# Performance work log

Measured on AMD Instinct MI355X. Metric: run time of the kernel, lower is better.

Reference implementation:

```python
import jax, jax.numpy as jnp
import numpy as np

N_NODES = 50000
N_EDGES = 600000
N_DISCRETE = 70
NH = N_DISCRETE - 6          # 64
EMB = 128                    # n_embedding
D = NH + EMB                 # 192, resdnn/cross input dim
RES_HID = 512                # l_hidden entries
N_RES = 2                    # len(l_hidden)
N_CROSS = 2
PRED_HID = (2 * NH + 512) // 2  # 320
NEG_SLOPE = 0.01


def setup_inputs() -> dict:
    key = jax.random.key(0)
    ks = jax.random.split(key, 24)
    def w(k, shape, fan_in):
        return (jax.random.normal(k, shape, jnp.float32) / np.sqrt(fan_in)).astype(jnp.float32)
    inp = {
        "discrete_x": jax.random.randint(ks[0], (N_NODES, N_DISCRETE), 0, 100, jnp.int64),
        "edge_index": jax.random.randint(ks[1], (2, N_EDGES), 0, N_NODES, jnp.int64),
        # graph embedding linear + 2 GCN layers
        "w_g0": w(ks[2], (NH, EMB), NH), "b_g0": jnp.zeros((EMB,), jnp.float32),
        "w_gcn1": w(ks[3], (EMB, EMB), EMB), "b_gcn1": jnp.zeros((EMB,), jnp.float32),
        "w_gcn2": w(ks[4], (EMB, EMB), EMB), "b_gcn2": jnp.zeros((EMB,), jnp.float32),
        # ResDNN: N_RES dim-preserving residual bottleneck blocks D->RES_HID->D
        "res_w1": w(ks[5], (N_RES, D, RES_HID), D), "res_b1": jnp.zeros((N_RES, RES_HID), jnp.float32),
        "res_w2": w(ks[6], (N_RES, RES_HID, D), RES_HID), "res_b2": jnp.zeros((N_RES, D), jnp.float32),
        # CrossNet: N_CROSS layers
        "cross_w": w(ks[7], (N_CROSS, D), D), "cross_b": jnp.zeros((N_CROSS, D), jnp.float32),
        # Prediction MLP: 2D -> PRED_HID -> 1, sigmoid
        "p_w1": w(ks[8], (2 * D, PRED_HID), 2 * D), "p_b1": jnp.zeros((PRED_HID,), jnp.float32),
        "p_w2": w(ks[9], (PRED_HID, 1), PRED_HID), "p_b2": jnp.zeros((1,), jnp.float32),
    }
    return inp


def _leaky(x):
    return jax.nn.leaky_relu(x, NEG_SLOPE)


def _gcn_conv(x, W, b, row, col, n):
    # PyG GCNConv: linear, then sym-normalized aggregation over A + I, then bias
    h = x @ W
    deg = jax.ops.segment_sum(jnp.ones(row.shape, x.dtype), col, num_segments=n) + 1.0
    dinv = jax.lax.rsqrt(deg)
    norm = dinv[row] * dinv[col]            # [E]
    msg = h[row] * norm[:, None]            # [E, EMB]  (largest intermediate)
    agg = jax.ops.segment_sum(msg, col, num_segments=n)
    agg = agg + h * (dinv * dinv)[:, None]  # self-loop contribution
    return agg + b


def reference(discrete_x, edge_index, w_g0, b_g0, w_gcn1, b_gcn1, w_gcn2, b_gcn2,
              res_w1, res_b1, res_w2, res_b2, cross_w, cross_b,
              p_w1, p_b1, p_w2, p_b2):
    n = discrete_x.shape[0]
    row, col = edge_index[0], edge_index[1]
    # DiscreteFeatureEmbeddingLayer: map n_discrete_features int cols -> nh float dims
    x_d = discrete_x[:, :NH].astype(jnp.float32)
    # graph branch
    x_g = _leaky(x_d @ w_g0 + b_g0)
    x_g = _leaky(_gcn_conv(x_g, w_gcn1, b_gcn1, row, col, n))
    x_g = _leaky(_gcn_conv(x_g, w_gcn2, b_gcn2, row, col, n))
    x = jnp.concatenate([x_d, x_g], axis=-1)  # [N, D]
    # ResDNN: residual bottleneck blocks
    x_deep = x
    for i in range(N_RES):
        h = _leaky(x_deep @ res_w1[i] + res_b1[i])
        x_deep = _leaky(x_deep + h @ res_w2[i] + res_b2[i])
    # CrossNet (DCN): x_{l+1} = x0 * (x_l . w_l) + b_l + x_l
    x0 = x
    x_cross = x
    for i in range(N_CROSS):
        xw = x_cross @ cross_w[i]            # [N]
        x_cross = x0 * xw[:, None] + cross_b[i] + x_cross
    z = jnp.concatenate([x_deep, x_cross], axis=-1)  # [N, 2D]
    h = _leaky(z @ p_w1 + p_b1)
    y = jax.nn.sigmoid(h @ p_w2 + p_b2)
    return y.squeeze(-1)
```

## Files before the change

### kernel.cpp

```cpp
#include <hip/hip_runtime.h>
#include <math.h>

constexpr int NCOLS   = 70;
constexpr int NH      = 64;
constexpr int EMB     = 128;
constexpr int DD      = 192;
constexpr int RES_HID = 512;
constexpr int PRED_HID= 320;

typedef _Float16 f16x8 __attribute__((ext_vector_type(8)));
typedef float    f32x4 __attribute__((ext_vector_type(4)));
#define MFMA16F(a,b,c) __builtin_amdgcn_mfma_f32_16x16x32_f16((a),(b),(c),0,0,0)

constexpr float LO_SCALE   = 4096.0f;
constexpr float LO_DESCALE = 1.0f/4096.0f;
constexpr float Z_SCALE    = 0.0625f;
constexpr float Z_DESCALE  = 16.0f;

__device__ __forceinline__ float leaky(float x){ return x > 0.f ? x : 0.01f*x; }

__global__ void k_hist(const int* __restrict__ col, int* __restrict__ cnt, int E){
  int e = blockIdx.x*256 + threadIdx.x;
  if (e < E) atomicAdd(&cnt[col[e]], 1);
}
__global__ void k_scanA(const int* __restrict__ cnt, int* __restrict__ bsum, int n){
  __shared__ int s;
  if (threadIdx.x == 0) s = 0;
  __syncthreads();
  int i = blockIdx.x*256 + threadIdx.x;
  int v = (i < n) ? cnt[i] : 0;
  #pragma unroll
  for (int o=32;o;o>>=1) v += __shfl_xor(v, o, 64);
  if ((threadIdx.x & 63) == 0) atomicAdd(&s, v);
  __syncthreads();
  if (threadIdx.x == 0) bsum[blockIdx.x] = s;
}
__global__ void k_scanB(int* bsum, int nb){
  __shared__ int s[256];
  __shared__ int carry;
  if (threadIdx.x == 0) carry = 0;
  __syncthreads();
  for (int start = 0; start < nb; start += 256){
    int i = start + threadIdx.x;
    int v = (i < nb) ? bsum[i] : 0;
    s[threadIdx.x] = v; __syncthreads();
    for (int o=1;o<256;o<<=1){
      int t = (threadIdx.x >= o) ? s[threadIdx.x-o] : 0;
      __syncthreads();
      s[threadIdx.x] += t; __syncthreads();
    }
    if (i < nb) bsum[i] = carry + s[threadIdx.x] - v;
    __syncthreads();
    if (threadIdx.x == 255) carry += s[255];
    __syncthreads();
  }
}
__global__ void k_scanC(const int* __restrict__ cnt, const int* __restrict__ bsum,
                        int* __restrict__ base, int* __restrict__ cursor,
                        float* __restrict__ dinv, int n, int E){
  __shared__ int s[256];
  int i = blockIdx.x*256 + threadIdx.x;
  int v = (i < n) ? cnt[i] : 0;
  s[threadIdx.x] = v; __syncthreads();
  for (int o=1;o<256;o<<=1){
    int t = (threadIdx.x >= o) ? s[threadIdx.x-o] : 0;
    __syncthreads();
    s[threadIdx.x] += t; __syncthreads();
  }
  if (i < n){
    int b = bsum[blockIdx.x] + s[threadIdx.x] - v;
    base[i] = b; cursor[i] = b;
    dinv[i] = rsqrtf((float)(v + 1));
  }
  if (i == n-1) base[n] = E;
}
__global__ void k_fill(const int* __restrict__ row, const int* __restrict__ col,
                       const float* __restrict__ dinv, int* __restrict__ cursor,
                       int2* __restrict__ ebin, int E){
  int e = blockIdx.x*256 + threadIdx.x;
  if (e < E){
    int r = row[e], c = col[e];
    int slot = atomicAdd(&cursor[c], 1);
    ebin[slot] = make_int2(r, __float_as_int(dinv[r]));
  }
}

__device__ __forceinline__ void pack_one(const float* __restrict__ W,
                                         _Float16* __restrict__ Wh, _Float16* __restrict__ Wl,
                                         int K, int N, int local){
  int k = local / N, nn = local - k*N;
  float v = W[local];
  _Float16 h = (_Float16)v;
  float lo = (v - (float)h)*LO_SCALE;
  int kc = k >> 5, r = k & 31;
  int lane = (nn & 15) | ((r >> 3) << 4);
  int j = r & 7;
  size_t dst = ((size_t)((nn >> 4)*(K >> 5) + kc) << 9) + lane*8 + j;
  Wh[dst] = h;
  Wl[dst] = (_Float16)lo;
}
__global__ void k_wprep_all(const float* res_w1, const float* res_w2, const float* p_w1,
                            const float* w_g0, const float* w_gcn1, const float* w_gcn2,
                            _Float16* wt1h, _Float16* wt1l, _Float16* wt2h, _Float16* wt2l,
                            _Float16* wph, _Float16* wpl, _Float16* wg0h, _Float16* wg0l,
                            _Float16* wg1h, _Float16* wg1l, _Float16* wg2h, _Float16* wg2l)
{
  int idx = blockIdx.x*256 + threadIdx.x;
  constexpr int SZ = DD*RES_HID;
  constexpr int PZ = 2*DD*PRED_HID;
  if (idx < SZ)                 pack_one(res_w1,           wt1h,      wt1l,      DD, RES_HID, idx);
  else if (idx < 2*SZ)          pack_one(res_w1 + SZ,      wt1h + SZ, wt1l + SZ, DD, RES_HID, idx - SZ);
  else if (idx < 3*SZ)          pack_one(res_w2,           wt2h,      wt2l,      RES_HID, DD, idx - 2*SZ);
  else if (idx < 4*SZ)          pack_one(res_w2 + SZ,      wt2h + SZ, wt2l + SZ, RES_HID, DD, idx - 3*SZ);
  else if (idx < 4*SZ + PZ)     pack_one(p_w1,             wph,       wpl,       2*DD, PRED_HID, idx - 4*SZ);
  else if (idx < 4*SZ + PZ + NH*EMB)
                                pack_one(w_g0,             wg0h,      wg0l,      NH, EMB, idx - 4*SZ - PZ);
  else if (idx < 4*SZ + PZ + NH*EMB + EMB*EMB)
                                pack_one(w_gcn1,           wg1h,      wg1l,      EMB, EMB, idx - 4*SZ - PZ - NH*EMB);
  else if (idx < 4*SZ + PZ + NH*EMB + 2*EMB*EMB)
                                pack_one(w_gcn2,           wg2h,      wg2l,      EMB, EMB, idx - 4*SZ - PZ - NH*EMB - EMB*EMB);
}

__global__ __launch_bounds__(256,3)
void k_embed_lin(const int* __restrict__ dx,
                 const _Float16* __restrict__ Wh, const _Float16* __restrict__ Wl,
                 const float* __restrict__ bias,
                 float* __restrict__ A,
                 float* __restrict__ out,
                 int n)
{
  constexpr int KS = 68;
  __shared__ __align__(16) _Float16 xh[32*KS];
  int i0 = blockIdx.x*32;
  for (int idx = threadIdx.x; idx < 32*NH; idx += 256){
    int t = idx >> 6, k = idx & 63;
    int i = i0 + t;
    float v = (i < n) ? (float)dx[(size_t)i*NCOLS + k] : 0.f;
    if (i < n) A[(size_t)i*DD + k] = v;
    xh[t*KS + k] = (_Float16)v;
  }
  __syncthreads();
  int wv = threadIdx.x >> 6, ln = threadIdx.x & 63;
  int cn = ln & 15, kg = ln >> 4;
  f16x8 A0h[2], A1h[2];
  #pragma unroll
  for (int kc=0;kc<2;kc++){
    int k0 = kc*32 + kg*8;
    A0h[kc] = *(const f16x8*)&xh[cn*KS + k0];
    A1h[kc] = *(const f16x8*)&xh[(16+cn)*KS + k0];
  }
  #pragma unroll
  for (int t=0;t<2;t++){
    int nt = wv*2 + t, n0 = nt*16;
    const _Float16* wbh = Wh + (((size_t)nt*2) << 9) + ln*8;
    const _Float16* wbl = Wl + (((size_t)nt*2) << 9) + ln*8;
    f32x4 acc0={0.f,0.f,0.f,0.f}, accL0={0.f,0.f,0.f,0.f};
    f32x4 acc1={0.f,0.f,0.f,0.f}, accL1={0.f,0.f,0.f,0.f};
    #pragma unroll
    for (int kc=0;kc<2;kc++){
      f16x8 bh = *(const f16x8*)(wbh + ((size_t)kc<<9));
      f16x8 bl = *(const f16x8*)(wbl + ((size_t)kc<<9));
      acc0  = MFMA16F(A0h[kc], bh, acc0);
      accL0 = MFMA16F(A0h[kc], bl, accL0);
      acc1  = MFMA16F(A1h[kc], bh, acc1);
      accL1 = MFMA16F(A1h[kc], bl, accL1);
    }
    float bb = bias[n0 + cn];
    #pragma unroll
    for (int r=0;r<4;r++){
      int ia = i0 + kg*4 + r, ib = ia + 16;
      float v0 = leaky(acc0[r] + accL0[r]*LO_DESCALE + bb);
      float v1 = leaky(acc1[r] + accL1[r]*LO_DESCALE + bb);
      if (ia < n) out[(size_t)ia*EMB + n0 + cn] = v0;
      if (ib < n) out[(size_t)ib*EMB + n0 + cn] = v1;
    }
  }
}

template<int KC>
__global__ __launch_bounds__(256,3)
void k_lin_mfma2(const float* __restrict__ X, int ldx,
                 const _Float16* __restrict__ Wh, const _Float16* __restrict__ Wl,
                 const float* __restrict__ bias,
                 float* __restrict__ out, int ldo, int ooff, int n, int act)
{
  constexpr int K  = KC*32;
  constexpr int KS = K + 4;
  __shared__ __align__(16) _Float16 xh[32*KS];
  __shared__ __align__(16) _Float16 xl[32*KS];
  int i0 = blockIdx.x*32;
  for (int idx = threadIdx.x; idx < 32*K; idx += 256){
    int t = idx / K, k = idx - t*K;
    int i = i0 + t;
    float v = (i < n) ? X[(size_t)i*ldx + k] : 0.f;
    _Float16 h = (_Float16)v;
    xh[t*KS + k] = h;
    xl[t*KS + k] = (_Float16)((v - (float)h)*LO_SCALE);
  }
  __syncthreads();
  int wv = threadIdx.x >> 6, ln = threadIdx.x & 63;
  int cn = ln & 15, kg = ln >> 4;
  f16x8 A0h[KC], A0l[KC], A1h[KC], A1l[KC];
  #pragma unroll
  for (int kc=0;kc<KC;kc++){
    int k0 = kc*32 + kg*8;
    A0h[kc] = *(const f16x8*)&xh[cn*KS + k0];
    A0l[kc] = *(const f16x8*)&xl[cn*KS + k0];
    A1h[kc] = *(const f16x8*)&xh[(16+cn)*KS + k0];
    A1l[kc] = *(const f16x8*)&xl[(16+cn)*KS + k0];
  }
  #pragma unroll
  for (int t=0;t<2;t++){
    int nt = wv*2 + t, n0 = nt*16;
    const _Float16* wbh = Wh + (((size_t)nt*KC) << 9) + ln*8;
    const _Float16* wbl = Wl + (((size_t)nt*KC) << 9) + ln*8;
    f32x4 acc0={0.f,0.f,0.f,0.f}, accL0={0.f,0.f,0.f,0.f};
    f32x4 acc1={0.f,0.f,0.f,0.f}, accL1={0.f,0.f,0.f,0.f};
    #pragma unroll
    for (int kc=0;kc<KC;kc++){
      f16x8 bh = *(const f16x8*)(wbh + ((size_t)kc<<9));
      f16x8 bl = *(const f16x8*)(wbl + ((size_t)kc<<9));
      acc0  = MFMA16F(A0h[kc], bh, acc0);
      accL0 = MFMA16F(A0l[kc], bh, accL0);
      accL0 = MFMA16F(A0h[kc], bl, accL0);
      acc1  = MFMA16F(A1h[kc], bh, acc1);
      accL1 = MFMA16F(A1l[kc], bh, accL1);
      accL1 = MFMA16F(A1h[kc], bl, accL1);
    }
    float bb = bias ? bias[n0 + cn] : 0.f;
    #pragma unroll
    for (int r=0;r<4;r++){
      int ia = i0 + kg*4 + r, ib = ia + 16;
      float v0 = acc0[r] + accL0[r]*LO_DESCALE + bb;
      float v1 = acc1[r] + accL1[r]*LO_DESCALE + bb;
      if (act){ v0 = leaky(v0); v1 = leaky(v1); }
      if (ia < n) out[(size_t)ia*ldo + ooff + n0 + cn] = v0;
      if (ib < n) out[(size_t)ib*ldo + ooff + n0 + cn] = v1;
    }
  }
}

__global__ void k_gather(const float* __restrict__ h, const float* __restrict__ dinv,
                         const int* __restrict__ base, const int2* __restrict__ ebin,
                         const float* __restrict__ bias, float* __restrict__ out,
                         int ldo, int ooff, int n)
{
  int node = blockIdx.x*4 + (threadIdx.x >> 6);
  int lane = threadIdx.x & 63;
  if (node >= n) return;
  int half = lane >> 5, l32 = lane & 31;
  int b0 = base[node], b1 = base[node+1];
  float dc = dinv[node];
  float4 acc = {0.f,0.f,0.f,0.f};
  for (int e = b0 + half; e < b1; e += 2){
    int2 ee = ebin[e];
    float4 hv = ((const float4*)(h + (size_t)ee.x*EMB))[l32];
    float dd = __int_as_float(ee.y);
    acc.x = fmaf(hv.x, dd, acc.x);
    acc.y = fmaf(hv.y, dd, acc.y);
    acc.z = fmaf(hv.z, dd, acc.z);
    acc.w = fmaf(hv.w, dd, acc.w);
  }
  acc.x += __shfl_xor(acc.x, 32, 64);
  acc.y += __shfl_xor(acc.y, 32, 64);
  acc.z += __shfl_xor(acc.z, 32, 64);
  acc.w += __shfl_xor(acc.w, 32, 64);
  float4 hc = ((const float4*)(h + (size_t)node*EMB))[l32];
  float4 bv = ((const float4*)bias)[l32];
  float4 res;
  res.x = leaky((acc.x + hc.x*dc)*dc + bv.x);
  res.y = leaky((acc.y + hc.y*dc)*dc + bv.y);
  res.z = leaky((acc.z + hc.z*dc)*dc + bv.z);
  res.w = leaky((acc.w + hc.w*dc)*dc + bv.w);
  if (half == 0)
    *(float4*)(out + (size_t)node*ldo + ooff + 4*l32) = res;
}

constexpr int XS = 196;
constexpr int HS = 516;

__global__ __launch_bounds__(256,2)
void k_resblock_mfma(const float* __restrict__ X,
                     const _Float16* __restrict__ W1h, const _Float16* __restrict__ W1l,
                     const float* __restrict__ b1,
                     const _Float16* __restrict__ W2h, const _Float16* __restrict__ W2l,
                     const float* __restrict__ b2,
                     float* __restrict__ out, int n)
{
  __shared__ __align__(16) _Float16 xh[32*XS];
  __shared__ __align__(16) _Float16 xl[32*XS];
  __shared__ __align__(16) _Float16 hh[32*HS];
  int i0 = blockIdx.x*32;
  for (int idx = threadIdx.x; idx < 32*DD; idx += 256){
    int t = idx / DD, k = idx - t*DD;
    int i = i0 + t;
    float v = (i < n) ? X[(size_t)i*DD + k] : 0.f;
    _Float16 h = (_Float16)v;
    xh[t*XS + k] = h;
    xl[t*XS + k] = (_Float16)((v - (float)h)*LO_SCALE);
  }
  __syncthreads();
  int wv = threadIdx.x >> 6, ln = threadIdx.x & 63;
  int cn = ln & 15, kg = ln >> 4;

  {
    f16x8 A0h[6], A0l[6], A1h[6], A1l[6];
    #pragma unroll
    for (int kc=0;kc<6;kc++){
      int k0 = kc*32 + kg*8;
      A0h[kc] = *(const f16x8*)&xh[cn*XS + k0];
      A0l[kc] = *(const f16x8*)&xl[cn*XS + k0];
      A1h[kc] = *(const f16x8*)&xh[(16+cn)*XS + k0];
      A1l[kc] = *(const f16x8*)&xl[(16+cn)*XS + k0];
    }
    float bias1[8];
    #pragma unroll
    for (int ct=0;ct<8;ct++) bias1[ct] = b1[(wv*8+ct)*16 + cn];
    const _Float16* pbh = W1h + ((size_t)(wv*8)*6 << 9) + ln*8;
    const _Float16* pbl = W1l + ((size_t)(wv*8)*6 << 9) + ln*8;
    f16x8 Bh[6], Bl[6];
    #pragma unroll
    for (int kc=0;kc<6;kc++){
      Bh[kc] = *(const f16x8*)(pbh + ((size_t)kc<<9));
      Bl[kc] = *(const f16x8*)(pbl + ((size_t)kc<<9));
    }
    #pragma unroll 1
    for (int ct = 0; ct < 8; ct++){
      f16x8 Bh2[6], Bl2[6];
      if (ct < 7){
        const _Float16* nh = pbh + ((size_t)((ct+1)*6) << 9);
        const _Float16* nl = pbl + ((size_t)((ct+1)*6) << 9);
        #pragma unroll
        for (int kc=0;kc<6;kc++){
          Bh2[kc] = *(const f16x8*)(nh + ((size_t)kc<<9));
          Bl2[kc] = *(const f16x8*)(nl + ((size_t)kc<<9));
        }
      }
      f32x4 acc0={0.f,0.f,0.f,0.f}, accL0={0.f,0.f,0.f,0.f};
      f32x4 acc1={0.f,0.f,0.f,0.f}, accL1={0.f,0.f,0.f,0.f};
      #pragma unroll
      for (int kc=0;kc<6;kc++){
        acc0  = MFMA16F(A0h[kc], Bh[kc], acc0);
        accL0 = MFMA16F(A0l[kc], Bh[kc], accL0);
        accL0 = MFMA16F(A0h[kc], Bl[kc], accL0);
        acc1  = MFMA16F(A1h[kc], Bh[kc], acc1);
        accL1 = MFMA16F(A1l[kc], Bh[kc], accL1);
        accL1 = MFMA16F(A1h[kc], Bl[kc], accL1);
      }
      int n0 = (wv*8+ct)*16;
      float bb = bias1[ct];
      #pragma unroll
      for (int r=0;r<4;r++){
        hh[(kg*4+r)*HS + n0 + cn]    = (_Float16)leaky(acc0[r] + accL0[r]*LO_DESCALE + bb);
        hh[(16+kg*4+r)*HS + n0 + cn] = (_Float16)leaky(acc1[r] + accL1[r]*LO_DESCALE + bb);
      }
      #pragma unroll
      for (int kc=0;kc<6;kc++){ Bh[kc]=Bh2[kc]; Bl[kc]=Bl2[kc]; }
    }
  }
  __syncthreads();

  {
    f32x4 acc[3][2], accL[3][2];
    #pragma unroll
    for (int c=0;c<3;c++){
      #pragma unroll
      for (int g=0;g<2;g++){
        acc[c][g]  = (f32x4){0.f,0.f,0.f,0.f};
        accL[c][g] = (f32x4){0.f,0.f,0.f,0.f};
      }
    }
    f16x8 B2h[3], B2l[3];
    #pragma unroll
    for (int c=0;c<3;c++){
      size_t off = ((size_t)((wv*3+c)*16) << 9) + ln*8;
      B2h[c] = *(const f16x8*)(W2h + off);
      B2l[c] = *(const f16x8*)(W2l + off);
    }
    #pragma unroll 1
    for (int kc=0;kc<16;kc++){
      f16x8 N2h[3], N2l[3];
      if (kc < 15){
        #pragma unroll
        for (int c=0;c<3;c++){
          size_t off = ((size_t)((wv*3+c)*16 + kc + 1) << 9) + ln*8;
          N2h[c] = *(const f16x8*)(W2h + off);
          N2l[c] = *(const f16x8*)(W2l + off);
        }
      }
      int k0 = kc*32 + kg*8;
      f16x8 a0 = *(const f16x8*)&hh[cn*HS + k0];
      f16x8 a1 = *(const f16x8*)&hh[(16+cn)*HS + k0];
      #pragma unroll
      for (int c=0;c<3;c++){
        acc[c][0]  = MFMA16F(a0, B2h[c], acc[c][0]);
        accL[c][0] = MFMA16F(a0, B2l[c], accL[c][0]);
        acc[c][1]  = MFMA16F(a1, B2h[c], acc[c][1]);
        accL[c][1] = MFMA16F(a1, B2l[c], accL[c][1]);
      }
      #pragma unroll
      for (int c=0;c<3;c++){ B2h[c]=N2h[c]; B2l[c]=N2l[c]; }
    }
    #pragma unroll
    for (int c=0;c<3;c++){
      int n0 = (wv*3+c)*16;
      float bb = b2[n0 + cn];
      #pragma unroll
      for (int r=0;r<4;r++){
        int m0 = kg*4 + r, m1 = 16 + kg*4 + r;
        float res0 = (float)xh[m0*XS + n0 + cn] + (float)xl[m0*XS + n0 + cn]*LO_DESCALE;
        float res1 = (float)xh[m1*XS + n0 + cn] + (float)xl[m1*XS + n0 + cn]*LO_DESCALE;
        int ia = i0 + m0, ib = i0 + m1;
        if (ia < n) out[(size_t)ia*DD + n0 + cn] = leaky(res0 + acc[c][0][r] + accL[c][0][r]*LO_DESCALE + bb);
        if (ib < n) out[(size_t)ib*DD + n0 + cn] = leaky(res1 + acc[c][1][r] + accL[c][1][r]*LO_DESCALE + bb);
      }
    }
  }
}

constexpr int ZS = 392;

__global__ __launch_bounds__(256,3)
void k_pred_mfma(const float* __restrict__ deep, const float* __restrict__ X0,
                 const float* __restrict__ cw, const float* __restrict__ cb,
                 const _Float16* __restrict__ Wh, const _Float16* __restrict__ Wl,
                 const float* __restrict__ b1,
                 const float* __restrict__ w2, const float* __restrict__ b2,
                 float* __restrict__ y, int n)
{
  __shared__ __align__(16) _Float16 zh[32*ZS];
  __shared__ __align__(16) _Float16 zl[32*ZS];
  __shared__ float sred[4][32];
  int i0 = blockIdx.x*32;
  for (int idx = threadIdx.x; idx < 32*DD; idx += 256){
    int t = idx / DD, k = idx - t*DD;
    int i = i0 + t;
    float v = (i < n) ? deep[(size_t)i*DD + k] : 0.f;
    v *= Z_SCALE;
    _Float16 h = (_Float16)v;
    zh[t*ZS + k] = h;
    zl[t*ZS + k] = (_Float16)((v - (float)h)*LO_SCALE);
  }
  int wv = threadIdx.x >> 6, ln = threadIdx.x & 63;
  for (int m = 0; m < 8; m++){
    int t = wv*8 + m;
    int node = i0 + t;
    float v0[3], xc[3];
    if (node < n){
      const float* xr = X0 + (size_t)node*DD;
      #pragma unroll
      for (int q=0;q<3;q++){ v0[q] = xr[ln + 64*q]; xc[q] = v0[q]; }
      #pragma unroll
      for (int l=0;l<2;l++){
        float p = 0.f;
        #pragma unroll
        for (int q=0;q<3;q++) p += xc[q]*cw[l*DD + ln + 64*q];
        #pragma unroll
        for (int off=32; off>0; off>>=1) p += __shfl_xor(p, off, 64);
        #pragma unroll
        for (int q=0;q<3;q++) xc[q] = v0[q]*p + cb[l*DD + ln + 64*q] + xc[q];
      }
    } else {
      #pragma unroll
      for (int q=0;q<3;q++) xc[q] = 0.f;
    }
    #pragma unroll
    for (int q=0;q<3;q++){
      float v = xc[q]*Z_SCALE;
      _Float16 h = (_Float16)v;
      zh[t*ZS + DD + ln + 64*q] = h;
      zl[t*ZS + DD + ln + 64*q] = (_Float16)((v - (float)h)*LO_SCALE);
    }
  }
  __syncthreads();
  int cn = ln & 15, kg = ln >> 4;
  float vs0[4] = {0.f,0.f,0.f,0.f};
  float vs1[4] = {0.f,0.f,0.f,0.f};
  #pragma unroll 1
  for (int ct = 0; ct < 5; ct++){
    int nt = wv*5 + ct;
    int n0 = nt*16;
    f32x4 acc0 = {0.f,0.f,0.f,0.f}, accL0 = {0.f,0.f,0.f,0.f};
    f32x4 acc1 = {0.f,0.f,0.f,0.f}, accL1 = {0.f,0.f,0.f,0.f};
    const _Float16* wbh = Wh + ((size_t)nt*12 << 9) + ln*8;
    const _Float16* wbl = Wl + ((size_t)nt*12 << 9) + ln*8;
    #pragma unroll 4
    for (int kc = 0; kc < 12; kc++){
      f16x8 bh = *(const f16x8*)(wbh + (kc << 9));
      f16x8 bl = *(const f16x8*)(wbl + (kc << 9));
      int k0 = kc*32 + kg*8;
      f16x8 a0h = *(const f16x8*)&zh[cn*ZS + k0];
      f16x8 a0l = *(const f16x8*)&zl[cn*ZS + k0];
      f16x8 a1h = *(const f16x8*)&zh[(16+cn)*ZS + k0];
      f16x8 a1l = *(const f16x8*)&zl[(16+cn)*ZS + k0];
      acc0  = MFMA16F(a0h, bh, acc0);
      accL0 = MFMA16F(a0l, bh, accL0);
      accL0 = MFMA16F(a0h, bl, accL0);
      acc1  = MFMA16F(a1h, bh, acc1);
      accL1 = MFMA16F(a1l, bh, accL1);
      accL1 = MFMA16F(a1h, bl, accL1);
    }
    float bb = b1[n0 + cn];
    float ww = w2[n0 + cn];
    #pragma unroll
    for (int r=0;r<4;r++){
      float v0 = (acc0[r] + accL0[r]*LO_DESCALE)*Z_DESCALE + bb;
      float v1 = (acc1[r] + accL1[r]*LO_DESCALE)*Z_DESCALE + bb;
      vs0[r] += leaky(v0)*ww;
      vs1[r] += leaky(v1)*ww;
    }
  }
  #pragma unroll
  for (int r=0;r<4;r++){
    #pragma unroll
    for (int off=1; off<16; off<<=1){
      vs0[r] += __shfl_xor(vs0[r], off, 64);
      vs1[r] += __shfl_xor(vs1[r], off, 64);
    }
  }
  if (cn == 0){
    #pragma unroll
    for (int r=0;r<4;r++){
      sred[wv][kg*4 + r]      = vs0[r];
      sred[wv][16 + kg*4 + r] = vs1[r];
    }
  }
  __syncthreads();
  if (threadIdx.x < 32){
    int m = threadIdx.x;
    float s = sred[0][m] + sred[1][m] + sred[2][m] + sred[3][m] + b2[0];
    int i = i0 + m;
    if (i < n) y[i] = 1.f/(1.f + expf(-s));
  }
}

extern "C" void kernel_launch(void* const* d_in, const int* in_sizes, int n_in,
                              void* d_out, int out_size, void* d_ws, size_t ws_size,
                              hipStream_t stream)
{
  const int*   dx      = (const int*)d_in[0];
  const int*   ei      = (const int*)d_in[1];
  const float* w_g0    = (const float*)d_in[2];
  const float* b_g0    = (const float*)d_in[3];
  const float* w_gcn1  = (const float*)d_in[4];
  const float* b_gcn1  = (const float*)d_in[5];
  const float* w_gcn2  = (const float*)d_in[6];
  const float* b_gcn2  = (const float*)d_in[7];
  const float* res_w1  = (const float*)d_in[8];
  const float* res_b1  = (const float*)d_in[9];
  const float* res_w2  = (const float*)d_in[10];
  const float* res_b2  = (const float*)d_in[11];
  const float* cross_w = (const float*)d_in[12];
  const float* cross_b = (const float*)d_in[13];
  const float* p_w1    = (const float*)d_in[14];
  const float* p_b1    = (const float*)d_in[15];
  const float* p_w2    = (const float*)d_in[16];
  const float* p_b2    = (const float*)d_in[17];
  float* y = (float*)d_out;

  int n = in_sizes[0] / NCOLS;
  int E = in_sizes[1] / 2;
  const int* row = ei;
  const int* col = ei + E;

  float* ws  = (float*)d_ws;
  float* A   = ws;
  float* B   = A  + (size_t)192*n;
  float* G   = B  + (size_t)192*n;
  float* E1  = G;
  float* E2v = G  + (size_t)128*n;
  float* dinv= G  + (size_t)256*n;
  int*  cnt    = (int*)(dinv + n);
  int*  base   = cnt + n;
  int*  cursor = base + n + 2;
  int*  bsum   = cursor + n;
  int2* ebin   = (int2*)((((uintptr_t)(bsum + 256)) + 15) & ~(uintptr_t)15);
  _Float16* wt1h = (_Float16*)((((uintptr_t)(ebin + E)) + 15) & ~(uintptr_t)15);
  _Float16* wt1l = wt1h + (size_t)2*RES_HID*DD;
  _Float16* wt2h = wt1l + (size_t)2*RES_HID*DD;
  _Float16* wt2l = wt2h + (size_t)2*RES_HID*DD;
  _Float16* wph  = wt2l + (size_t)2*RES_HID*DD;
  _Float16* wpl  = wph  + (size_t)PRED_HID*2*DD;
  _Float16* wg0h = wpl  + (size_t)PRED_HID*2*DD;
  _Float16* wg0l = wg0h + (size_t)NH*EMB;
  _Float16* wg1h = wg0l + (size_t)NH*EMB;
  _Float16* wg1l = wg1h + (size_t)EMB*EMB;
  _Float16* wg2h = wg1l + (size_t)EMB*EMB;
  _Float16* wg2l = wg2h + (size_t)EMB*EMB;

  dim3 blk(256);
  int nb = (n + 255)/256;

  {
    int total = 4*DD*RES_HID + 2*DD*PRED_HID + NH*EMB + 2*EMB*EMB;
    k_wprep_all<<<(total+255)/256, blk, 0, stream>>>(res_w1, res_w2, p_w1, w_g0, w_gcn1, w_gcn2,
                                                     wt1h, wt1l, wt2h, wt2l, wph, wpl,
                                                     wg0h, wg0l, wg1h, wg1l, wg2h, wg2l);
  }

  hipMemsetAsync(cnt, 0, (size_t)n*sizeof(int), stream);
  k_hist <<<(E+255)/256, blk, 0, stream>>>(col, cnt, E);
  k_scanA<<<nb, blk, 0, stream>>>(cnt, bsum, n);
  k_scanB<<<1, blk, 0, stream>>>(bsum, nb);
  k_scanC<<<nb, blk, 0, stream>>>(cnt, bsum, base, cursor, dinv, n, E);
  k_fill <<<(E+255)/256, blk, 0, stream>>>(row, col, dinv, cursor, ebin, E);

  int rbt = (n + 31)/32;
  k_embed_lin<<<rbt, blk, 0, stream>>>(dx, wg0h, wg0l, b_g0, A, E1, n);
  k_lin_mfma2<4><<<rbt, blk, 0, stream>>>(E1, EMB, wg1h, wg1l, nullptr, E2v, EMB, 0, n, 0);
  k_gather  <<<(n+3)/4, blk, 0, stream>>>(E2v, dinv, base, ebin, b_gcn1, E1, EMB, 0, n);
  k_lin_mfma2<4><<<rbt, blk, 0, stream>>>(E1, EMB, wg2h, wg2l, nullptr, E2v, EMB, 0, n, 0);
  k_gather  <<<(n+3)/4, blk, 0, stream>>>(E2v, dinv, base, ebin, b_gcn2, A, DD, NH, n);
  k_resblock_mfma<<<rbt, blk, 0, stream>>>(A, wt1h, wt1l, res_b1,
                                           wt2h, wt2l, res_b2, B, n);
  k_resblock_mfma<<<rbt, blk, 0, stream>>>(B, wt1h + (size_t)DD*RES_HID, wt1l + (size_t)DD*RES_HID,
                                           res_b1 + RES_HID,
                                           wt2h + (size_t)DD*RES_HID, wt2l + (size_t)DD*RES_HID,
                                           res_b2 + DD, B, n);
  k_pred_mfma<<<rbt, blk, 0, stream>>>(B, A, cross_w, cross_b, wph, wpl, p_b1, p_w2, p_b2, y, n);
}
```

Measured before the change: 615.4 us.

## Fuse both residual blocks and prediction head into one kernel

Merges the two resblock launches and the prediction/cross kernel into a single kernel that keeps each 32-row tile in shared memory as hi/lo fp16 across stages. This removes the global write and re-read of the intermediate deep activations B, along with two launches. In exchange, shared memory per block grows and 24 floats are held in registers while the z buffers reuse the same space. That may lower occupancy, and the launch bound for the prediction stage drops from 3 to 2 blocks.

Measured after the change: 620.9 us. Within noise of the previous version (+0.9%).

```diff
diff --git a/kernel.cpp b/kernel.cpp
--- a/kernel.cpp
+++ b/kernel.cpp
@@ -125,9 +125,7 @@
 void k_embed_lin(const int* __restrict__ dx,
                  const _Float16* __restrict__ Wh, const _Float16* __restrict__ Wl,
                  const float* __restrict__ bias,
-                 float* __restrict__ A,
-                 float* __restrict__ out,
-                 int n)
+                 float* __restrict__ A, float* __restrict__ out, int n)
 {
   constexpr int KS = 68;
   __shared__ __align__(16) _Float16 xh[32*KS];
@@ -278,23 +276,31 @@
 
 constexpr int XS = 196;
 constexpr int HS = 516;
+constexpr int ZS = 392;
 
 __global__ __launch_bounds__(256,2)
-void k_resblock_mfma(const float* __restrict__ X,
-                     const _Float16* __restrict__ W1h, const _Float16* __restrict__ W1l,
-                     const float* __restrict__ b1,
-                     const _Float16* __restrict__ W2h, const _Float16* __restrict__ W2l,
-                     const float* __restrict__ b2,
-                     float* __restrict__ out, int n)
+void k_mega(const float* __restrict__ X0,
+            const _Float16* __restrict__ w11h, const _Float16* __restrict__ w11l, const float* __restrict__ b11,
+            const _Float16* __restrict__ w12h, const _Float16* __restrict__ w12l, const float* __restrict__ b12,
+            const _Float16* __restrict__ w21h, const _Float16* __restrict__ w21l, const float* __restrict__ b21,
+            const _Float16* __restrict__ w22h, const _Float16* __restrict__ w22l, const float* __restrict__ b22,
+            const float* __restrict__ cw, const float* __restrict__ cb,
+            const _Float16* __restrict__ wph, const _Float16* __restrict__ wpl,
+            const float* __restrict__ pb1, const float* __restrict__ pw2, const float* __restrict__ pb2,
+            float* __restrict__ y, int n)
 {
-  __shared__ __align__(16) _Float16 xh[32*XS];
-  __shared__ __align__(16) _Float16 xl[32*XS];
-  __shared__ __align__(16) _Float16 hh[32*HS];
+  __shared__ __align__(16) _Float16 smem[32*(2*XS + HS)];
+  __shared__ float sred[4][32];
+  _Float16* xh = smem;
+  _Float16* xl = smem + 32*XS;
+  _Float16* hh = smem + 64*XS;
+  _Float16* zh = smem;
+  _Float16* zl = smem + 32*ZS;
   int i0 = blockIdx.x*32;
   for (int idx = threadIdx.x; idx < 32*DD; idx += 256){
     int t = idx / DD, k = idx - t*DD;
     int i = i0 + t;
-    float v = (i < n) ? X[(size_t)i*DD + k] : 0.f;
+    float v = (i < n) ? X0[(size_t)i*DD + k] : 0.f;
     _Float16 h = (_Float16)v;
     xh[t*XS + k] = h;
     xl[t*XS + k] = (_Float16)((v - (float)h)*LO_SCALE);
@@ -303,145 +309,152 @@
   int wv = threadIdx.x >> 6, ln = threadIdx.x & 63;
   int cn = ln & 15, kg = ln >> 4;
 
+  #pragma unroll 1
+  for (int rb = 0; rb < 2; rb++){
+    const _Float16* W1h = rb ? w21h : w11h;
+    const _Float16* W1l = rb ? w21l : w11l;
+    const float*    b1  = rb ? b21  : b11;
+    const _Float16* W2h = rb ? w22h : w12h;
+    const _Float16* W2l = rb ? w22l : w12l;
+    const float*    b2  = rb ? b22  : b12;
+    {
+      f16x8 A0h[6], A0l[6], A1h[6], A1l[6];
+      #pragma unroll
+      for (int kc=0;kc<6;kc++){
+        int k0 = kc*32 + kg*8;
+        A0h[kc] = *(const f16x8*)&xh[cn*XS + k0];
+        A0l[kc] = *(const f16x8*)&xl[cn*XS + k0];
+        A1h[kc] = *(const f16x8*)&xh[(16+cn)*XS + k0];
+        A1l[kc] = *(const f16x8*)&xl[(16+cn)*XS + k0];
+      }
+      float bias1[8];
+      #pragma unroll
+      for (int ct=0;ct<8;ct++) bias1[ct] = b1[(wv*8+ct)*16 + cn];
+      const _Float16* pbh = W1h + ((size_t)(wv*8)*6 << 9) + ln*8;
+      const _Float16* pbl = W1l + ((size_t)(wv*8)*6 << 9) + ln*8;
+      f16x8 Bh[6], Bl[6];
+      #pragma unroll
+      for (int kc=0;kc<6;kc++){
+        Bh[kc] = *(const f16x8*)(pbh + ((size_t)kc<<9));
+        Bl[kc] = *(const f16x8*)(pbl + ((size_t)kc<<9));
+      }
+      #pragma unroll 1
+      for (int ct = 0; ct < 8; ct++){
+        f16x8 Bh2[6], Bl2[6];
+        if (ct < 7){
+          const _Float16* nh = pbh + ((size_t)((ct+1)*6) << 9);
+          const _Float16* nl = pbl + ((size_t)((ct+1)*6) << 9);
+          #pragma unroll
+          for (int kc=0;kc<6;kc++){
+            Bh2[kc] = *(const f16x8*)(nh + ((size_t)kc<<9));
+            Bl2[kc] = *(const f16x8*)(nl + ((size_t)kc<<9));
+          }
+        }
+        f32x4 acc0={0.f,0.f,0.f,0.f}, accL0={0.f,0.f,0.f,0.f};
+        f32x4 acc1={0.f,0.f,0.f,0.f}, accL1={0.f,0.f,0.f,0.f};
+        #pragma unroll
+        for (int kc=0;kc<6;kc++){
+          acc0  = MFMA16F(A0h[kc], Bh[kc], acc0);
+          accL0 = MFMA16F(A0l[kc], Bh[kc], accL0);
+          accL0 = MFMA16F(A0h[kc], Bl[kc], accL0);
+          acc1  = MFMA16F(A1h[kc], Bh[kc], acc1);
+          accL1 = MFMA16F(A1l[kc], Bh[kc], accL1);
+          accL1 = MFMA16F(A1h[kc], Bl[kc], accL1);
+        }
+        int n0 = (wv*8+ct)*16;
+        float bb = bias1[ct];
+        #pragma unroll
+        for (int r=0;r<4;r++){
+          hh[(kg*4+r)*HS + n0 + cn]    = (_Float16)leaky(acc0[r] + accL0[r]*LO_DESCALE + bb);
+          hh[(16+kg*4+r)*HS + n0 + cn] = (_Float16)leaky(acc1[r] + accL1[r]*LO_DESCALE + bb);
+        }
+        #pragma unroll
+        for (int kc=0;kc<6;kc++){ Bh[kc]=Bh2[kc]; Bl[kc]=Bl2[kc]; }
+      }
+    }
+    __syncthreads();
+    {
+      f32x4 acc[3][2], accL[3][2];
+      #pragma unroll
+      for (int c=0;c<3;c++){
+        #pragma unroll
+        for (int g=0;g<2;g++){
+          acc[c][g]  = (f32x4){0.f,0.f,0.f,0.f};
+          accL[c][g] = (f32x4){0.f,0.f,0.f,0.f};
+        }
+      }
+      f16x8 B2h[3], B2l[3];
+      #pragma unroll
+      for (int c=0;c<3;c++){
+        size_t off = ((size_t)((wv*3+c)*16) << 9) + ln*8;
+        B2h[c] = *(const f16x8*)(W2h + off);
+        B2l[c] = *(const f16x8*)(W2l + off);
+      }
+      #pragma unroll 1
+      for (int kc=0;kc<16;kc++){
+        f16x8 N2h[3], N2l[3];
+        if (kc < 15){
+          #pragma unroll
+          for (int c=0;c<3;c++){
+            size_t off = ((size_t)((wv*3+c)*16 + kc + 1) << 9) + ln*8;
+            N2h[c] = *(const f16x8*)(W2h + off);
+            N2l[c] = *(const f16x8*)(W2l + off);
+          }
+        }
+        int k0 = kc*32 + kg*8;
+        f16x8 a0 = *(const f16x8*)&hh[cn*HS + k0];
+        f16x8 a1 = *(const f16x8*)&hh[(16+cn)*HS + k0];
+        #pragma unroll
+        for (int c=0;c<3;c++){
+          acc[c][0]  = MFMA16F(a0, B2h[c], acc[c][0]);
+          accL[c][0] = MFMA16F(a0, B2l[c], accL[c][0]);
+          acc[c][1]  = MFMA16F(a1, B2h[c], acc[c][1]);
+          accL[c][1] = MFMA16F(a1, B2l[c], accL[c][1]);
+        }
+        #pragma unroll
+        for (int c=0;c<3;c++){ B2h[c]=N2h[c]; B2l[c]=N2l[c]; }
+      }
+      #pragma unroll
+      for (int c=0;c<3;c++){
+        int n0 = (wv*3+c)*16;
+        float bb = b2[n0 + cn];
+        #pragma unroll
+        for (int r=0;r<4;r++){
+          int m0 = kg*4 + r, m1 = 16 + kg*4 + r;
+          float res0 = (float)xh[m0*XS + n0 + cn] + (float)xl[m0*XS + n0 + cn]*LO_DESCALE;
+          float res1 = (float)xh[m1*XS + n0 + cn] + (float)xl[m1*XS + n0 + cn]*LO_DESCALE;
+          float o0 = leaky(res0 + acc[c][0][r] + accL[c][0][r]*LO_DESCALE + bb);
+          float o1 = leaky(res1 + acc[c][1][r] + accL[c][1][r]*LO_DESCALE + bb);
+          _Float16 h0 = (_Float16)o0, h1 = (_Float16)o1;
+          xh[m0*XS + n0 + cn] = h0;
+          xl[m0*XS + n0 + cn] = (_Float16)((o0 - (float)h0)*LO_SCALE);
+          xh[m1*XS + n0 + cn] = h1;
+          xl[m1*XS + n0 + cn] = (_Float16)((o1 - (float)h1)*LO_SCALE);
+        }
+      }
+    }
+    __syncthreads();
+  }
+
+  float dv[24];
   {
-    f16x8 A0h[6], A0l[6], A1h[6], A1l[6];
-    #pragma unroll
-    for (int kc=0;kc<6;kc++){
-      int k0 = kc*32 + kg*8;
-      A0h[kc] = *(const f16x8*)&xh[cn*XS + k0];
-      A0l[kc] = *(const f16x8*)&xl[cn*XS + k0];
-      A1h[kc] = *(const f16x8*)&xh[(16+cn)*XS + k0];
-      A1l[kc] = *(const f16x8*)&xl[(16+cn)*XS + k0];
-    }
-    float bias1[8];
-    #pragma unroll
-    for (int ct=0;ct<8;ct++) bias1[ct] = b1[(wv*8+ct)*16 + cn];
-    const _Float16* pbh = W1h + ((size_t)(wv*8)*6 << 9) + ln*8;
-    const _Float16* pbl = W1l + ((size_t)(wv*8)*6 << 9) + ln*8;
-    f16x8 Bh[6], Bl[6];
-    #pragma unroll
-    for (int kc=0;kc<6;kc++){
-      Bh[kc] = *(const f16x8*)(pbh + ((size_t)kc<<9));
-      Bl[kc] = *(const f16x8*)(pbl + ((size_t)kc<<9));
-    }
-    #pragma unroll 1
-    for (int ct = 0; ct < 8; ct++){
-      f16x8 Bh2[6], Bl2[6];
-      if (ct < 7){
-        const _Float16* nh = pbh + ((size_t)((ct+1)*6) << 9);
-        const _Float16* nl = pbl + ((size_t)((ct+1)*6) << 9);
-        #pragma unroll
-        for (int kc=0;kc<6;kc++){
-          Bh2[kc] = *(const f16x8*)(nh + ((size_t)kc<<9));
-          Bl2[kc] = *(const f16x8*)(nl + ((size_t)kc<<9));
-        }
-      }
-      f32x4 acc0={0.f,0.f,0.f,0.f}, accL0={0.f,0.f,0.f,0.f};
-      f32x4 acc1={0.f,0.f,0.f,0.f}, accL1={0.f,0.f,0.f,0.f};
-      #pragma unroll
-      for (int kc=0;kc<6;kc++){
-        acc0  = MFMA16F(A0h[kc], Bh[kc], acc0);
-        accL0 = MFMA16F(A0l[kc], Bh[kc], accL0);
-        accL0 = MFMA16F(A0h[kc], Bl[kc], accL0);
-        acc1  = MFMA16F(A1h[kc], Bh[kc], acc1);
-        accL1 = MFMA16F(A1l[kc], Bh[kc], accL1);
-        accL1 = MFMA16F(A1h[kc], Bl[kc], accL1);
-      }
-      int n0 = (wv*8+ct)*16;
-      float bb = bias1[ct];
-      #pragma unroll
-      for (int r=0;r<4;r++){
-        hh[(kg*4+r)*HS + n0 + cn]    = (_Float16)leaky(acc0[r] + accL0[r]*LO_DESCALE + bb);
-        hh[(16+kg*4+r)*HS + n0 + cn] = (_Float16)leaky(acc1[r] + accL1[r]*LO_DESCALE + bb);
-      }
-      #pragma unroll
-      for (int kc=0;kc<6;kc++){ Bh[kc]=Bh2[kc]; Bl[kc]=Bl2[kc]; }
-    }
-  }
-  __syncthreads();
-
+    int c = 0;
+    for (int idx = threadIdx.x; idx < 32*DD; idx += 256){
+      int t = idx / DD, k = idx - t*DD;
+      dv[c++] = (float)xh[t*XS + k] + (float)xl[t*XS + k]*LO_DESCALE;
+    }
+  }
+  __syncthreads();
   {
-    f32x4 acc[3][2], accL[3][2];
-    #pragma unroll
-    for (int c=0;c<3;c++){
-      #pragma unroll
-      for (int g=0;g<2;g++){
-        acc[c][g]  = (f32x4){0.f,0.f,0.f,0.f};
-        accL[c][g] = (f32x4){0.f,0.f,0.f,0.f};
-      }
-    }
-    f16x8 B2h[3], B2l[3];
-    #pragma unroll
-    for (int c=0;c<3;c++){
-      size_t off = ((size_t)((wv*3+c)*16) << 9) + ln*8;
-      B2h[c] = *(const f16x8*)(W2h + off);
-      B2l[c] = *(const f16x8*)(W2l + off);
-    }
-    #pragma unroll 1
-    for (int kc=0;kc<16;kc++){
-      f16x8 N2h[3], N2l[3];
-      if (kc < 15){
-        #pragma unroll
-        for (int c=0;c<3;c++){
-          size_t off = ((size_t)((wv*3+c)*16 + kc + 1) << 9) + ln*8;
-          N2h[c] = *(const f16x8*)(W2h + off);
-          N2l[c] = *(const f16x8*)(W2l + off);
-        }
-      }
-      int k0 = kc*32 + kg*8;
-      f16x8 a0 = *(const f16x8*)&hh[cn*HS + k0];
-      f16x8 a1 = *(const f16x8*)&hh[(16+cn)*HS + k0];
-      #pragma unroll
-      for (int c=0;c<3;c++){
-        acc[c][0]  = MFMA16F(a0, B2h[c], acc[c][0]);
-        accL[c][0] = MFMA16F(a0, B2l[c], accL[c][0]);
-        acc[c][1]  = MFMA16F(a1, B2h[c], acc[c][1]);
-        accL[c][1] = MFMA16F(a1, B2l[c], accL[c][1]);
-      }
-      #pragma unroll
-      for (int c=0;c<3;c++){ B2h[c]=N2h[c]; B2l[c]=N2l[c]; }
-    }
-    #pragma unroll
-    for (int c=0;c<3;c++){
-      int n0 = (wv*3+c)*16;
-      float bb = b2[n0 + cn];
-      #pragma unroll
-      for (int r=0;r<4;r++){
-        int m0 = kg*4 + r, m1 = 16 + kg*4 + r;
-        float res0 = (float)xh[m0*XS + n0 + cn] + (float)xl[m0*XS + n0 + cn]*LO_DESCALE;
-        float res1 = (float)xh[m1*XS + n0 + cn] + (float)xl[m1*XS + n0 + cn]*LO_DESCALE;
-        int ia = i0 + m0, ib = i0 + m1;
-        if (ia < n) out[(size_t)ia*DD + n0 + cn] = leaky(res0 + acc[c][0][r] + accL[c][0][r]*LO_DESCALE + bb);
-        if (ib < n) out[(size_t)ib*DD + n0 + cn] = leaky(res1 + acc[c][1][r] + accL[c][1][r]*LO_DESCALE + bb);
-      }
-    }
-  }
-}
-
-constexpr int ZS = 392;
-
-__global__ __launch_bounds__(256,3)
-void k_pred_mfma(const float* __restrict__ deep, const float* __restrict__ X0,
-                 const float* __restrict__ cw, const float* __restrict__ cb,
-                 const _Float16* __restrict__ Wh, const _Float16* __restrict__ Wl,
-                 const float* __restrict__ b1,
-                 const float* __restrict__ w2, const float* __restrict__ b2,
-                 float* __restrict__ y, int n)
-{
-  __shared__ __align__(16) _Float16 zh[32*ZS];
-  __shared__ __align__(16) _Float16 zl[32*ZS];
-  __shared__ float sred[4][32];
-  int i0 = blockIdx.x*32;
-  for (int idx = threadIdx.x; idx < 32*DD; idx += 256){
-    int t = idx / DD, k = idx - t*DD;
-    int i = i0 + t;
-    float v = (i < n) ? deep[(size_t)i*DD + k] : 0.f;
-    v *= Z_SCALE;
-    _Float16 h = (_Float16)v;
-    zh[t*ZS + k] = h;
-    zl[t*ZS + k] = (_Float16)((v - (float)h)*LO_SCALE);
-  }
-  int wv = threadIdx.x >> 6, ln = threadIdx.x & 63;
+    int c = 0;
+    for (int idx = threadIdx.x; idx < 32*DD; idx += 256){
+      int t = idx / DD, k = idx - t*DD;
+      float v = dv[c++]*Z_SCALE;
+      _Float16 h = (_Float16)v;
+      zh[t*ZS + k] = h;
+      zl[t*ZS + k] = (_Float16)((v - (float)h)*LO_SCALE);
+    }
+  }
   for (int m = 0; m < 8; m++){
     int t = wv*8 + m;
     int node = i0 + t;
@@ -473,7 +486,6 @@
     }
   }
   __syncthreads();
-  int cn = ln & 15, kg = ln >> 4;
   float vs0[4] = {0.f,0.f,0.f,0.f};
   float vs1[4] = {0.f,0.f,0.f,0.f};
   #pragma unroll 1
@@ -482,8 +494,8 @@
     int n0 = nt*16;
     f32x4 acc0 = {0.f,0.f,0.f,0.f}, accL0 = {0.f,0.f,0.f,0.f};
     f32x4 acc1 = {0.f,0.f,0.f,0.f}, accL1 = {0.f,0.f,0.f,0.f};
-    const _Float16* wbh = Wh + ((size_t)nt*12 << 9) + ln*8;
-    const _Float16* wbl = Wl + ((size_t)nt*12 << 9) + ln*8;
+    const _Float16* wbh = wph + ((size_t)nt*12 << 9) + ln*8;
+    const _Float16* wbl = wpl + ((size_t)nt*12 << 9) + ln*8;
     #pragma unroll 4
     for (int kc = 0; kc < 12; kc++){
       f16x8 bh = *(const f16x8*)(wbh + (kc << 9));
@@ -500,8 +512,8 @@
       accL1 = MFMA16F(a1l, bh, accL1);
       accL1 = MFMA16F(a1h, bl, accL1);
     }
-    float bb = b1[n0 + cn];
-    float ww = w2[n0 + cn];
+    float bb = pb1[n0 + cn];
+    float ww = pw2[n0 + cn];
     #pragma unroll
     for (int r=0;r<4;r++){
       float v0 = (acc0[r] + accL0[r]*LO_DESCALE)*Z_DESCALE + bb;
@@ -528,7 +540,7 @@
   __syncthreads();
   if (threadIdx.x < 32){
     int m = threadIdx.x;
-    float s = sred[0][m] + sred[1][m] + sred[2][m] + sred[3][m] + b2[0];
+    float s = sred[0][m] + sred[1][m] + sred[2][m] + sred[3][m] + pb2[0];
     int i = i0 + m;
     if (i < n) y[i] = 1.f/(1.f + expf(-s));
   }
@@ -611,11 +623,12 @@
   k_gather  <<<(n+3)/4, blk, 0, stream>>>(E2v, dinv, base, ebin, b_gcn1, E1, EMB, 0, n);
   k_lin_mfma2<4><<<rbt, blk, 0, stream>>>(E1, EMB, wg2h, wg2l, nullptr, E2v, EMB, 0, n, 0);
   k_gather  <<<(n+3)/4, blk, 0, stream>>>(E2v, dinv, base, ebin, b_gcn2, A, DD, NH, n);
-  k_resblock_mfma<<<rbt, blk, 0, stream>>>(A, wt1h, wt1l, res_b1,
-                                           wt2h, wt2l, res_b2, B, n);
-  k_resblock_mfma<<<rbt, blk, 0, stream>>>(B, wt1h + (size_t)DD*RES_HID, wt1l + (size_t)DD*RES_HID,
-                                           res_b1 + RES_HID,
-                                           wt2h + (size_t)DD*RES_HID, wt2l + (size_t)DD*RES_HID,
-                                           res_b2 + DD, B, n);
-  k_pred_mfma<<<rbt, blk, 0, stream>>>(B, A, cross_w, cross_b, wph, wpl, p_b1, p_w2, p_b2, y, n);
-}
+  size_t SZ = (size_t)DD*RES_HID;
+  k_mega<<<rbt, blk, 0, stream>>>(A,
+                                  wt1h, wt1l, res_b1,
+                                  wt2h, wt2l, res_b2,
+                                  wt1h + SZ, wt1l + SZ, res_b1 + RES_HID,
+                                  wt2h + SZ, wt2l + SZ, res_b2 + DD,
+                                  cross_w, cross_b,
+                                  wph, wpl, p_b1, p_w2, p_b2, y, n);
+}
```
